# Kernel tuning notes

Hardware: AMD Instinct MI355X
Metric: run time of the kernel (lower is better)

Reference implementation:

```python
import jax, jax.numpy as jnp
import numpy as np
import math

D_MODEL = 1024
NHEAD = 16
HEAD_DIM = D_MODEL // NHEAD  # 64
FREQ = 10000.0


def _rope(x, freq=FREQ):
    # x: [B, H, S, D] with D even. Matches RotaryEmbedding.apply:
    # thetas = exp(-2*log(freq)*(i//2)/D) for i in [0, D/2)
    S, D = x.shape[-2], x.shape[-1]
    pos = jnp.arange(S, dtype=x.dtype)                       # [S]
    idx = jnp.arange(D // 2) // 2                            # floor(i/2)
    thetas = jnp.exp((-2.0 * math.log(freq) / D) * idx.astype(x.dtype))  # [D/2]
    ang = pos[:, None] * thetas[None, :]                     # [S, D/2]
    cos, sin = jnp.cos(ang), jnp.sin(ang)
    x2 = x.reshape(*x.shape[:-1], D // 2, 2)
    x0, x1 = x2[..., 0], x2[..., 1]
    out = jnp.stack([x0 * cos - x1 * sin, x0 * sin + x1 * cos], axis=-1)
    return out.reshape(x.shape)


def setup_inputs() -> dict:
    key = jax.random.key(0)
    k1, k2, k3, k4, k5 = jax.random.split(key, 5)
    B, S = 2, 2048
    scale = 1.0 / math.sqrt(D_MODEL)
    return {
        "embeddings": jax.random.normal(k1, (B, S, D_MODEL), dtype=jnp.float32),
        "W_qkv": jax.random.normal(k2, (D_MODEL, 3 * D_MODEL), dtype=jnp.float32) * scale,
        "b_qkv": jnp.zeros((3 * D_MODEL,), dtype=jnp.float32),
        "W_o": jax.random.normal(k4, (D_MODEL, D_MODEL), dtype=jnp.float32) * scale,
        "b_o": jnp.zeros((D_MODEL,), dtype=jnp.float32),
    }


def reference(embeddings, W_qkv, b_qkv, W_o, b_o):
    B, S, _ = embeddings.shape
    qkv = embeddings @ W_qkv + b_qkv                          # [B,S,3*D]
    q, k, v = jnp.split(qkv, 3, axis=-1)

    def split_heads(t):  # [B,S,D] -> [B,H,S,hd]
        return t.reshape(B, S, NHEAD, HEAD_DIM).transpose(0, 2, 1, 3)

    q, k, v = split_heads(q), split_heads(k), split_heads(v)
    q = _rope(q)
    k = _rope(k)

    scores = jnp.einsum("bhqd,bhkd->bhqk", q, k) / math.sqrt(HEAD_DIM)
    attn = jax.nn.softmax(scores, axis=-1)
    heads = jnp.einsum("bhqk,bhkd->bhqd", attn, v)            # [B,H,S,hd]
    out = heads.transpose(0, 2, 1, 3).reshape(B, S, D_MODEL)
    return out @ W_o + b_o
```

## Files before the change

kernel.cpp:

```cpp
#include <hip/hip_runtime.h>
#include <hip/hip_bf16.h>
#include <math.h>

typedef __bf16 bf16;
typedef __bf16 bf16x4 __attribute__((ext_vector_type(4)));
typedef __bf16 bf16x8 __attribute__((ext_vector_type(8)));
typedef float f32x4 __attribute__((ext_vector_type(4)));

#define DEV static __device__ __forceinline__

#define SS 2048
#define HH 16
#define HD 64

DEV void load_lds16(const bf16* g, bf16* l) {
  __builtin_amdgcn_global_load_lds(
      (const __attribute__((address_space(1))) unsigned int*)g,
      (__attribute__((address_space(3))) unsigned int*)l, 16, 0, 0);
}

#define MFMA(a, b, c) __builtin_amdgcn_mfma_f32_16x16x32_bf16(a, b, c, 0, 0, 0)

__global__ __launch_bounds__(256) void k_prep(
    const float* __restrict__ emb, bf16* __restrict__ Xb,
    const float* __restrict__ Wqkv, bf16* __restrict__ Wqt,
    const float* __restrict__ Wo, bf16* __restrict__ Wot) {
  __shared__ float tt[32][33];
  int bid = blockIdx.x;
  if (bid < 4096) {
    int i = (bid * 256 + threadIdx.x) * 4;
    float4 v = *reinterpret_cast<const float4*>(emb + i);
    bf16x4 o = {(bf16)v.x, (bf16)v.y, (bf16)v.z, (bf16)v.w};
    *reinterpret_cast<bf16x4*>(Xb + i) = o;
    return;
  }
  const float* in;
  bf16* out;
  int R = 1024, C, ctile, rtile;
  if (bid < 7168) {
    in = Wqkv; out = Wqt; C = 3072;
    int idx = bid - 4096; ctile = idx % 96; rtile = idx / 96;
  } else {
    in = Wo; out = Wot; C = 1024;
    int idx = bid - 7168; ctile = idx & 31; rtile = idx >> 5;
  }
  int tx = threadIdx.x & 31, ty = threadIdx.x >> 5;
#pragma unroll
  for (int i = 0; i < 4; ++i)
    tt[ty + 8 * i][tx] = in[(rtile * 32 + ty + 8 * i) * C + ctile * 32 + tx];
  __syncthreads();
#pragma unroll
  for (int i = 0; i < 4; ++i) {
    int oc = ctile * 32 + ty + 8 * i;
    out[oc * R + rtile * 32 + tx] = (bf16)tt[tx][ty + 8 * i];
  }
}

__global__ __launch_bounds__(512) void k_gemm1(
    const bf16* __restrict__ A, const bf16* __restrict__ Bt,
    const float* __restrict__ bias, bf16* __restrict__ Qo,
    bf16* __restrict__ Ko, bf16* __restrict__ Vo) {
  __shared__ bf16 As[2][16384];
  __shared__ bf16 Bs[2][16384];
  int wg = blockIdx.x;
  int xcd = wg & 7, idx = wg >> 3;
  int wgid = xcd * 24 + idx;
  int bm = wgid & 15, bn = wgid >> 4;
  int t = threadIdx.x, w = t >> 6, l = t & 63;
  int wm = w >> 2, wn = w & 3;
  int fr = l & 15, fg = l >> 4;
  const bf16* Ab = A + bm * 256 * 1024;
  const bf16* Bb = Bt + bn * 256 * 1024;
  int trow = t >> 3;
  const bf16* sA = Ab + trow * 1024 + (((t & 7) ^ (trow & 7)) * 8);
  const bf16* sB = Bb + trow * 1024 + (((t & 7) ^ (trow & 7)) * 8);
  int dst0 = (w << 9);
#pragma unroll
  for (int j = 0; j < 4; ++j) {
    load_lds16(sA + j * 65536, &As[0][j * 4096 + dst0]);
    load_lds16(sB + j * 65536, &Bs[0][j * 4096 + dst0]);
  }
  f32x4 acc[8][4];
#pragma unroll
  for (int mi = 0; mi < 8; ++mi)
#pragma unroll
    for (int ni = 0; ni < 4; ++ni) acc[mi][ni] = (f32x4){0.f, 0.f, 0.f, 0.f};
  int xo = fr & 7;
  __syncthreads();
  for (int kt = 0; kt < 16; ++kt) {
    const bf16* Asb = &As[kt & 1][0];
    const bf16* Bsb = &Bs[kt & 1][0];
    bf16* An = &As[(kt & 1) ^ 1][0];
    bf16* Bn = &Bs[(kt & 1) ^ 1][0];
    bool st = kt < 15;
    int ko = (kt + 1) * 64;
    bf16x8 av[4], bv[4];
    if (st) {
      load_lds16(sA + ko, &An[dst0]);
      load_lds16(sA + 65536 + ko, &An[4096 + dst0]);
    }
#pragma unroll
    for (int ni = 0; ni < 4; ++ni)
      bv[ni] = *(const bf16x8*)(Bsb + (wn * 64 + ni * 16 + fr) * 64 + (fg ^ xo) * 8);
#pragma unroll
    for (int mi = 0; mi < 4; ++mi)
      av[mi] = *(const bf16x8*)(Asb + (wm * 128 + mi * 16 + fr) * 64 + (fg ^ xo) * 8);
    __builtin_amdgcn_s_setprio(1);
#pragma unroll
    for (int mi = 0; mi < 4; ++mi)
#pragma unroll
      for (int ni = 0; ni < 4; ++ni)
        acc[mi][ni] = MFMA(av[mi], bv[ni], acc[mi][ni]);
    __builtin_amdgcn_s_setprio(0);
    if (st) {
      load_lds16(sA + 131072 + ko, &An[8192 + dst0]);
      load_lds16(sA + 196608 + ko, &An[12288 + dst0]);
    }
#pragma unroll
    for (int mi = 0; mi < 4; ++mi)
      av[mi] = *(const bf16x8*)(Asb + (wm * 128 + (mi + 4) * 16 + fr) * 64 + (fg ^ xo) * 8);
    __builtin_amdgcn_s_setprio(1);
#pragma unroll
    for (int mi = 0; mi < 4; ++mi)
#pragma unroll
      for (int ni = 0; ni < 4; ++ni)
        acc[mi + 4][ni] = MFMA(av[mi], bv[ni], acc[mi + 4][ni]);
    __builtin_amdgcn_s_setprio(0);
    if (st) {
      load_lds16(sB + ko, &Bn[dst0]);
      load_lds16(sB + 65536 + ko, &Bn[4096 + dst0]);
    }
#pragma unroll
    for (int ni = 0; ni < 4; ++ni)
      bv[ni] = *(const bf16x8*)(Bsb + (wn * 64 + ni * 16 + fr) * 64 + ((4 + fg) ^ xo) * 8);
#pragma unroll
    for (int mi = 0; mi < 4; ++mi)
      av[mi] = *(const bf16x8*)(Asb + (wm * 128 + mi * 16 + fr) * 64 + ((4 + fg) ^ xo) * 8);
    __builtin_amdgcn_s_setprio(1);
#pragma unroll
    for (int mi = 0; mi < 4; ++mi)
#pragma unroll
      for (int ni = 0; ni < 4; ++ni)
        acc[mi][ni] = MFMA(av[mi], bv[ni], acc[mi][ni]);
    __builtin_amdgcn_s_setprio(0);
    if (st) {
      load_lds16(sB + 131072 + ko, &Bn[8192 + dst0]);
      load_lds16(sB + 196608 + ko, &Bn[12288 + dst0]);
    }
#pragma unroll
    for (int mi = 0; mi < 4; ++mi)
      av[mi] = *(const bf16x8*)(Asb + (wm * 128 + (mi + 4) * 16 + fr) * 64 + ((4 + fg) ^ xo) * 8);
    __builtin_amdgcn_s_setprio(1);
#pragma unroll
    for (int mi = 0; mi < 4; ++mi)
#pragma unroll
      for (int ni = 0; ni < 4; ++ni)
        acc[mi + 4][ni] = MFMA(av[mi], bv[ni], acc[mi + 4][ni]);
    __builtin_amdgcn_s_setprio(0);
    __syncthreads();
  }
#pragma unroll
  for (int mi = 0; mi < 8; ++mi)
#pragma unroll
    for (int ni = 0; ni < 4; ++ni) {
      int gc = bn * 256 + wn * 64 + ni * 16 + fr;
      int sec = gc >> 10, cc = gc & 1023;
      bf16* dst = sec == 0 ? Qo : (sec == 1 ? Ko : Vo);
      int h = cc >> 6, d = cc & 63;
      float bb = bias[gc];
      int gr0 = bm * 256 + wm * 128 + mi * 16 + fg * 4;
#pragma unroll
      for (int r = 0; r < 4; ++r) {
        int gr = gr0 + r;
        int b = gr >> 11, s = gr & 2047;
        dst[((b * HH + h) * SS + s) * HD + d] = (bf16)(acc[mi][ni][r] + bb);
      }
    }
}

DEV void gemm_core(const bf16* __restrict__ Ab, const bf16* __restrict__ Bb,
                   bf16* As, bf16* Bs, int w, int l, f32x4 acc[4][4]) {
  int fr = l & 15, fg = l >> 4;
  int wr = (w >> 1) * 64, wc = (w & 1) * 64;
  for (int kt = 0; kt < 16; ++kt) {
#pragma unroll
    for (int i = 0; i < 4; ++i) {
      int blk = w * 4 + i;
      const bf16* ga = Ab + (blk * 8 + (l >> 3)) * 1024 + kt * 64 + (l & 7) * 8;
      const bf16* gb = Bb + (blk * 8 + (l >> 3)) * 1024 + kt * 64 + (l & 7) * 8;
      load_lds16(ga, As + blk * 512);
      load_lds16(gb, Bs + blk * 512);
    }
    __syncthreads();
#pragma unroll
    for (int kk = 0; kk < 2; ++kk) {
      bf16x8 af[4], bfv[4];
#pragma unroll
      for (int mi = 0; mi < 4; ++mi)
        af[mi] = *(const bf16x8*)(As + (wr + mi * 16 + fr) * 64 + kk * 32 + fg * 8);
#pragma unroll
      for (int ni = 0; ni < 4; ++ni)
        bfv[ni] = *(const bf16x8*)(Bs + (wc + ni * 16 + fr) * 64 + kk * 32 + fg * 8);
#pragma unroll
      for (int mi = 0; mi < 4; ++mi)
#pragma unroll
        for (int ni = 0; ni < 4; ++ni)
          acc[mi][ni] = __builtin_amdgcn_mfma_f32_16x16x32_bf16(
              af[mi], bfv[ni], acc[mi][ni], 0, 0, 0);
    }
    __syncthreads();
  }
}

__global__ __launch_bounds__(256) void k_gemm2(
    const bf16* __restrict__ A, const bf16* __restrict__ Bt,
    const float* __restrict__ bias, float* __restrict__ out) {
  __shared__ bf16 As[128 * 64], Bs[128 * 64];
  int wg = blockIdx.x;
  int bm = wg & 31, bn = wg >> 5;
  int t = threadIdx.x, w = t >> 6, l = t & 63;
  f32x4 acc[4][4];
#pragma unroll
  for (int mi = 0; mi < 4; ++mi)
#pragma unroll
    for (int ni = 0; ni < 4; ++ni) acc[mi][ni] = (f32x4){0.f, 0.f, 0.f, 0.f};
  gemm_core(A + bm * 128 * 1024, Bt + bn * 128 * 1024, As, Bs, w, l, acc);
  int fr = l & 15, fg = l >> 4;
  int wr = (w >> 1) * 64, wc = (w & 1) * 64;
#pragma unroll
  for (int mi = 0; mi < 4; ++mi)
#pragma unroll
    for (int ni = 0; ni < 4; ++ni) {
      int gc = bn * 128 + wc + ni * 16 + fr;
      float bb = bias[gc];
      int gr0 = bm * 128 + wr + mi * 16 + fg * 4;
#pragma unroll
      for (int r = 0; r < 4; ++r)
        out[(gr0 + r) * 1024 + gc] = acc[mi][ni][r] + bb;
    }
}

__global__ void k_rope(bf16* __restrict__ Qb, bf16* __restrict__ Kb) {
  int t = blockIdx.x * 256 + threadIdx.x;
  bf16* buf = (t >> 19) ? Kb : Qb;
  float qs = (t >> 19) ? 1.0f : 0.125f;
  int g = t & 524287;
  int j = g & 7;
  int s = (g >> 3) & 2047;
  bf16* p = buf + (long long)g * 8;
  const float CN = -0.28782313662425572f;
  float th0 = __expf(CN * (float)(2 * j));
  float th1 = __expf(CN * (float)(2 * j + 1));
  float sp = (float)s;
  float s0, c0, s1, c1;
  sincosf(sp * th0, &s0, &c0);
  sincosf(sp * th1, &s1, &c1);
  bf16x8 v = *(bf16x8*)p;
  float x[8];
#pragma unroll
  for (int i = 0; i < 8; ++i) x[i] = (float)v[i];
  float o[8];
  o[0] = x[0] * c0 - x[1] * s0; o[1] = x[0] * s0 + x[1] * c0;
  o[2] = x[2] * c0 - x[3] * s0; o[3] = x[2] * s0 + x[3] * c0;
  o[4] = x[4] * c1 - x[5] * s1; o[5] = x[4] * s1 + x[5] * c1;
  o[6] = x[6] * c1 - x[7] * s1; o[7] = x[6] * s1 + x[7] * c1;
  bf16x8 ov;
#pragma unroll
  for (int i = 0; i < 8; ++i) ov[i] = (bf16)(o[i] * qs);
  *(bf16x8*)p = ov;
}

__global__ void k_trV(const bf16* __restrict__ V, bf16* __restrict__ Vt) {
  __shared__ bf16 t[64][66];
  int st = blockIdx.x, bh = blockIdx.y;
  const bf16* vb = V + (long long)bh * SS * HD;
  bf16* ob = Vt + (long long)bh * HD * SS;
  int tx = threadIdx.x & 63, ty = threadIdx.x >> 6;
#pragma unroll
  for (int i = 0; i < 16; ++i)
    t[ty + 4 * i][tx] = vb[(st * 64 + ty + 4 * i) * 64 + tx];
  __syncthreads();
#pragma unroll
  for (int i = 0; i < 16; ++i) {
    int dR = ty + 4 * i;
    ob[dR * SS + st * 64 + tx] = t[tx][dR];
  }
}

__global__ __launch_bounds__(512) void k_attn(
    const bf16* __restrict__ Q, const bf16* __restrict__ K,
    const bf16* __restrict__ Vt, bf16* __restrict__ Hd) {
  __shared__ bf16 KVs[2][8192];
  __shared__ bf16 plds[8][16][72];
  int bid = blockIdx.x;
  int x = bid & 7, rr = bid >> 3;
  int bh = x * 4 + (rr & 3);
  int qt = rr >> 2;
  int b = bh >> 4, h = bh & 15;
  int t = threadIdx.x, w = t >> 6, l = t & 63;
  int fr = l & 15, fg = l >> 4;
  const bf16* Qb = Q + (long long)bh * SS * HD;
  const bf16* Kb = K + (long long)bh * SS * HD;
  const bf16* Vb = Vt + (long long)bh * HD * SS;
  bool isK = w < 4;
  int stride = isK ? 64 : 2048;
  int wrow = (isK ? w : (w - 4)) * 16 + (l >> 3);
  const bf16* src = (isK ? Kb : Vb) + wrow * stride + ((l & 7) ^ (l >> 3)) * 8;
  int adv = isK ? 4096 : 64;
  int dbase = w * 1024;

  int q0 = qt * 128 + w * 16;
  bf16x8 qf0 = *(const bf16x8*)(Qb + (q0 + fr) * 64 + fg * 8);
  bf16x8 qf1 = *(const bf16x8*)(Qb + (q0 + fr) * 64 + 32 + fg * 8);
  f32x4 acc[4];
#pragma unroll
  for (int db = 0; db < 4; ++db) acc[db] = (f32x4){0.f, 0.f, 0.f, 0.f};
  float ssum = 0.f;
  const f32x4 zero = {0.f, 0.f, 0.f, 0.f};
  int xo = fr & 7;

  load_lds16(src, &KVs[0][dbase]);
  load_lds16(src + 8 * stride, &KVs[0][dbase + 512]);
  src += adv;
  __syncthreads();

  for (int it = 0; it < 32; ++it) {
    int buf = it & 1;
    if (it < 31) {
      load_lds16(src, &KVs[buf ^ 1][dbase]);
      load_lds16(src + 8 * stride, &KVs[buf ^ 1][dbase + 512]);
      src += adv;
    }
    const bf16* Ks = &KVs[buf][0];
    const bf16* Vs = &KVs[buf][4096];
    f32x4 stl[4];
    __builtin_amdgcn_s_setprio(1);
#pragma unroll
    for (int ks = 0; ks < 4; ++ks) {
      bf16x8 k0 = *(const bf16x8*)(Ks + (ks * 16 + fr) * 64 + (fg ^ xo) * 8);
      bf16x8 k1 = *(const bf16x8*)(Ks + (ks * 16 + fr) * 64 + ((4 + fg) ^ xo) * 8);
      stl[ks] = MFMA(k0, qf0, zero);
      stl[ks] = MFMA(k1, qf1, stl[ks]);
    }
    __builtin_amdgcn_s_setprio(0);
    float ps = 0.f;
#pragma unroll
    for (int ks = 0; ks < 4; ++ks) {
      bf16x4 pb;
#pragma unroll
      for (int r = 0; r < 4; ++r) {
        float p = __expf(stl[ks][r] - 16.0f);
        ps += p;
        pb[r] = (bf16)p;
      }
      *(bf16x4*)&plds[w][fr][ks * 16 + fg * 4] = pb;
    }
    ssum += ps;
    bf16x8 pf0 = *(const bf16x8*)&plds[w][fr][fg * 8];
    bf16x8 pf1 = *(const bf16x8*)&plds[w][fr][32 + fg * 8];
    __builtin_amdgcn_s_setprio(1);
#pragma unroll
    for (int db = 0; db < 4; ++db) {
      bf16x8 vf0 = *(const bf16x8*)(Vs + (db * 16 + fr) * 64 + (fg ^ xo) * 8);
      bf16x8 vf1 = *(const bf16x8*)(Vs + (db * 16 + fr) * 64 + ((4 + fg) ^ xo) * 8);
      acc[db] = MFMA(vf0, pf0, acc[db]);
      acc[db] = MFMA(vf1, pf1, acc[db]);
    }
    __builtin_amdgcn_s_setprio(0);
    __syncthreads();
  }
  float sv = ssum;
  sv += __shfl_xor(sv, 16);
  sv += __shfl_xor(sv, 32);
  float inv = 1.0f / sv;
  int s = q0 + fr;
#pragma unroll
  for (int db = 0; db < 4; ++db) {
    bf16x4 ob;
#pragma unroll
    for (int r = 0; r < 4; ++r) ob[r] = (bf16)(acc[db][r] * inv);
    *(bf16x4*)(Hd + ((long long)(b * SS + s)) * 1024 + h * 64 + db * 16 + fg * 4) = ob;
  }
}

extern "C" void kernel_launch(void* const* d_in, const int* in_sizes, int n_in,
                              void* d_out, int out_size, void* d_ws, size_t ws_size,
                              hipStream_t stream) {
  const float* emb = (const float*)d_in[0];
  const float* Wqkv = (const float*)d_in[1];
  const float* bqkv = (const float*)d_in[2];
  const float* Wo = (const float*)d_in[3];
  const float* bo = (const float*)d_in[4];
  float* out = (float*)d_out;
  char* ws = (char*)d_ws;
  bf16* Xb  = (bf16*)(ws);
  bf16* Wqt = (bf16*)(ws + 8388608);
  bf16* Wot = (bf16*)(ws + 14680064);
  bf16* Qb  = (bf16*)(ws + 16777216);
  bf16* Kb  = (bf16*)(ws + 25165824);
  bf16* Vb  = (bf16*)(ws + 33554432);
  bf16* Vt  = (bf16*)(ws + 41943040);
  bf16* Hd  = (bf16*)(ws + 50331648);

  hipLaunchKernelGGL(k_prep, dim3(8192), dim3(256), 0, stream, emb, Xb, Wqkv, Wqt, Wo, Wot);
  hipLaunchKernelGGL(k_gemm1, dim3(192), dim3(512), 0, stream, Xb, Wqt, bqkv, Qb, Kb, Vb);
  hipLaunchKernelGGL(k_rope, dim3(4096), dim3(256), 0, stream, Qb, Kb);
  hipLaunchKernelGGL(k_trV, dim3(32, 32), dim3(256), 0, stream, Vb, Vt);
  hipLaunchKernelGGL(k_attn, dim3(512), dim3(512), 0, stream, Qb, Kb, Vt, Hd);
  hipLaunchKernelGGL(k_gemm2, dim3(256), dim3(256), 0, stream, Hd, Wot, bo, out);
}
```

Baseline: 138.4 us.

## Restructure QKV GEMM pipeline, remap tiles per XCD, use exp2 softmax

The QKV GEMM now issues the whole next-stage prefetch up front and places explicit s_barrier, waitcnt and sched_barrier fences around each MFMA phase instead of spreading loads between phases. Block-to-tile mapping is changed so each XCD covers a 4x6 rectangle of tiles, meant to improve L2 reuse. The attention kernel folds log2(e) into the Q scale so it can call exp2f instead of __expf, and it unrolls the KV loop by two with a fixed buffer index. These aim to cut instruction overhead and improve overlap and cache locality, but the extra barriers may add stalls.

```diff
diff --git a/kernel.cpp b/kernel.cpp
--- a/kernel.cpp
+++ b/kernel.cpp
@@ -64,8 +64,8 @@
   __shared__ bf16 Bs[2][16384];
   int wg = blockIdx.x;
   int xcd = wg & 7, idx = wg >> 3;
-  int wgid = xcd * 24 + idx;
-  int bm = wgid & 15, bn = wgid >> 4;
+  int bm = (xcd & 3) * 4 + (idx & 3);
+  int bn = (xcd >> 2) * 6 + (idx >> 2);
   int t = threadIdx.x, w = t >> 6, l = t & 63;
   int wm = w >> 2, wn = w & 3;
   int fr = l & 15, fg = l >> 4;
@@ -75,36 +75,42 @@
   const bf16* sA = Ab + trow * 1024 + (((t & 7) ^ (trow & 7)) * 8);
   const bf16* sB = Bb + trow * 1024 + (((t & 7) ^ (trow & 7)) * 8);
   int dst0 = (w << 9);
-#pragma unroll
-  for (int j = 0; j < 4; ++j) {
-    load_lds16(sA + j * 65536, &As[0][j * 4096 + dst0]);
-    load_lds16(sB + j * 65536, &Bs[0][j * 4096 + dst0]);
-  }
+  int xo = fr & 7;
+
+#define G1_STAGE(buf, ko)                                         \
+  do {                                                            \
+    _Pragma("unroll")                                             \
+    for (int j = 0; j < 4; ++j) {                                 \
+      load_lds16(sA + j * 65536 + (ko), &As[buf][j * 4096 + dst0]); \
+      load_lds16(sB + j * 65536 + (ko), &Bs[buf][j * 4096 + dst0]); \
+    }                                                             \
+  } while (0)
+
   f32x4 acc[8][4];
 #pragma unroll
   for (int mi = 0; mi < 8; ++mi)
 #pragma unroll
     for (int ni = 0; ni < 4; ++ni) acc[mi][ni] = (f32x4){0.f, 0.f, 0.f, 0.f};
-  int xo = fr & 7;
-  __syncthreads();
+
+  G1_STAGE(0, 0);
+  asm volatile("s_waitcnt vmcnt(0)" ::: "memory");
+  __builtin_amdgcn_s_barrier();
+
   for (int kt = 0; kt < 16; ++kt) {
-    const bf16* Asb = &As[kt & 1][0];
-    const bf16* Bsb = &Bs[kt & 1][0];
-    bf16* An = &As[(kt & 1) ^ 1][0];
-    bf16* Bn = &Bs[(kt & 1) ^ 1][0];
-    bool st = kt < 15;
-    int ko = (kt + 1) * 64;
+    int p = kt & 1;
+    const bf16* Asb = &As[p][0];
+    const bf16* Bsb = &Bs[p][0];
+    if (kt < 15) G1_STAGE(p ^ 1, (kt + 1) * 64);
     bf16x8 av[4], bv[4];
-    if (st) {
-      load_lds16(sA + ko, &An[dst0]);
-      load_lds16(sA + 65536 + ko, &An[4096 + dst0]);
-    }
 #pragma unroll
     for (int ni = 0; ni < 4; ++ni)
       bv[ni] = *(const bf16x8*)(Bsb + (wn * 64 + ni * 16 + fr) * 64 + (fg ^ xo) * 8);
 #pragma unroll
     for (int mi = 0; mi < 4; ++mi)
       av[mi] = *(const bf16x8*)(Asb + (wm * 128 + mi * 16 + fr) * 64 + (fg ^ xo) * 8);
+    __builtin_amdgcn_s_barrier();
+    asm volatile("s_waitcnt lgkmcnt(0)" ::: "memory");
+    __builtin_amdgcn_sched_barrier(0);
     __builtin_amdgcn_s_setprio(1);
 #pragma unroll
     for (int mi = 0; mi < 4; ++mi)
@@ -112,13 +118,13 @@
       for (int ni = 0; ni < 4; ++ni)
         acc[mi][ni] = MFMA(av[mi], bv[ni], acc[mi][ni]);
     __builtin_amdgcn_s_setprio(0);
-    if (st) {
-      load_lds16(sA + 131072 + ko, &An[8192 + dst0]);
-      load_lds16(sA + 196608 + ko, &An[12288 + dst0]);
-    }
+    __builtin_amdgcn_s_barrier();
 #pragma unroll
     for (int mi = 0; mi < 4; ++mi)
       av[mi] = *(const bf16x8*)(Asb + (wm * 128 + (mi + 4) * 16 + fr) * 64 + (fg ^ xo) * 8);
+    __builtin_amdgcn_s_barrier();
+    asm volatile("s_waitcnt lgkmcnt(0)" ::: "memory");
+    __builtin_amdgcn_sched_barrier(0);
     __builtin_amdgcn_s_setprio(1);
 #pragma unroll
     for (int mi = 0; mi < 4; ++mi)
@@ -126,16 +132,16 @@
       for (int ni = 0; ni < 4; ++ni)
         acc[mi + 4][ni] = MFMA(av[mi], bv[ni], acc[mi + 4][ni]);
     __builtin_amdgcn_s_setprio(0);
-    if (st) {
-      load_lds16(sB + ko, &Bn[dst0]);
-      load_lds16(sB + 65536 + ko, &Bn[4096 + dst0]);
-    }
+    __builtin_amdgcn_s_barrier();
 #pragma unroll
     for (int ni = 0; ni < 4; ++ni)
       bv[ni] = *(const bf16x8*)(Bsb + (wn * 64 + ni * 16 + fr) * 64 + ((4 + fg) ^ xo) * 8);
 #pragma unroll
     for (int mi = 0; mi < 4; ++mi)
       av[mi] = *(const bf16x8*)(Asb + (wm * 128 + mi * 16 + fr) * 64 + ((4 + fg) ^ xo) * 8);
+    __builtin_amdgcn_s_barrier();
+    asm volatile("s_waitcnt lgkmcnt(0)" ::: "memory");
+    __builtin_amdgcn_sched_barrier(0);
     __builtin_amdgcn_s_setprio(1);
 #pragma unroll
     for (int mi = 0; mi < 4; ++mi)
@@ -143,13 +149,13 @@
       for (int ni = 0; ni < 4; ++ni)
         acc[mi][ni] = MFMA(av[mi], bv[ni], acc[mi][ni]);
     __builtin_amdgcn_s_setprio(0);
-    if (st) {
-      load_lds16(sB + 131072 + ko, &Bn[8192 + dst0]);
-      load_lds16(sB + 196608 + ko, &Bn[12288 + dst0]);
-    }
+    __builtin_amdgcn_s_barrier();
 #pragma unroll
     for (int mi = 0; mi < 4; ++mi)
       av[mi] = *(const bf16x8*)(Asb + (wm * 128 + (mi + 4) * 16 + fr) * 64 + ((4 + fg) ^ xo) * 8);
+    __builtin_amdgcn_s_barrier();
+    asm volatile("s_waitcnt lgkmcnt(0)" ::: "memory");
+    __builtin_amdgcn_sched_barrier(0);
     __builtin_amdgcn_s_setprio(1);
 #pragma unroll
     for (int mi = 0; mi < 4; ++mi)
@@ -157,7 +163,9 @@
       for (int ni = 0; ni < 4; ++ni)
         acc[mi + 4][ni] = MFMA(av[mi], bv[ni], acc[mi + 4][ni]);
     __builtin_amdgcn_s_setprio(0);
-    __syncthreads();
+    asm volatile("s_waitcnt vmcnt(0)" ::: "memory");
+    __builtin_amdgcn_sched_barrier(0);
+    __builtin_amdgcn_s_barrier();
   }
 #pragma unroll
   for (int mi = 0; mi < 8; ++mi)
@@ -176,6 +184,7 @@
         dst[((b * HH + h) * SS + s) * HD + d] = (bf16)(acc[mi][ni][r] + bb);
       }
     }
+#undef G1_STAGE
 }
 
 DEV void gemm_core(const bf16* __restrict__ Ab, const bf16* __restrict__ Bb,
@@ -243,7 +252,7 @@
 __global__ void k_rope(bf16* __restrict__ Qb, bf16* __restrict__ Kb) {
   int t = blockIdx.x * 256 + threadIdx.x;
   bf16* buf = (t >> 19) ? Kb : Qb;
-  float qs = (t >> 19) ? 1.0f : 0.125f;
+  float qs = (t >> 19) ? 1.0f : 0.18033688011112042f;
   int g = t & 524287;
   int j = g & 7;
   int s = (g >> 3) & 2047;
@@ -319,54 +328,61 @@
   const f32x4 zero = {0.f, 0.f, 0.f, 0.f};
   int xo = fr & 7;
 
-  load_lds16(src, &KVs[0][dbase]);
-  load_lds16(src + 8 * stride, &KVs[0][dbase + 512]);
-  src += adv;
+#define ATTN_STAGE(BUF)                              \
+  do {                                               \
+    load_lds16(src, &KVs[BUF][dbase]);               \
+    load_lds16(src + 8 * stride, &KVs[BUF][dbase + 512]); \
+    src += adv;                                      \
+  } while (0)
+
+#define ATTN_COMPUTE(BUF)                                                    \
+  do {                                                                       \
+    const bf16* Ks = &KVs[BUF][0];                                           \
+    const bf16* Vs = &KVs[BUF][4096];                                        \
+    f32x4 stl[4];                                                            \
+    __builtin_amdgcn_s_setprio(1);                                           \
+    _Pragma("unroll")                                                        \
+    for (int ks = 0; ks < 4; ++ks) {                                         \
+      bf16x8 k0 = *(const bf16x8*)(Ks + (ks * 16 + fr) * 64 + (fg ^ xo) * 8);\
+      bf16x8 k1 = *(const bf16x8*)(Ks + (ks * 16 + fr) * 64 + ((4 + fg) ^ xo) * 8); \
+      stl[ks] = MFMA(k0, qf0, zero);                                         \
+      stl[ks] = MFMA(k1, qf1, stl[ks]);                                      \
+    }                                                                        \
+    __builtin_amdgcn_s_setprio(0);                                           \
+    float ps = 0.f;                                                          \
+    _Pragma("unroll")                                                        \
+    for (int ks = 0; ks < 4; ++ks) {                                         \
+      bf16x4 pb;                                                             \
+      _Pragma("unroll")                                                      \
+      for (int r = 0; r < 4; ++r) {                                          \
+        float p = exp2f(stl[ks][r] - 23.083120654223414f);                   \
+        ps += p;                                                             \
+        pb[r] = (bf16)p;                                                     \
+      }                                                                      \
+      *(bf16x4*)&plds[w][fr][ks * 16 + fg * 4] = pb;                         \
+    }                                                                        \
+    ssum += ps;                                                              \
+    bf16x8 pf0 = *(const bf16x8*)&plds[w][fr][fg * 8];                       \
+    bf16x8 pf1 = *(const bf16x8*)&plds[w][fr][32 + fg * 8];                  \
+    __builtin_amdgcn_s_setprio(1);                                           \
+    _Pragma("unroll")                                                        \
+    for (int db = 0; db < 4; ++db) {                                         \
+      bf16x8 vf0 = *(const bf16x8*)(Vs + (db * 16 + fr) * 64 + (fg ^ xo) * 8); \
+      bf16x8 vf1 = *(const bf16x8*)(Vs + (db * 16 + fr) * 64 + ((4 + fg) ^ xo) * 8); \
+      acc[db] = MFMA(vf0, pf0, acc[db]);                                     \
+      acc[db] = MFMA(vf1, pf1, acc[db]);                                     \
+    }                                                                        \
+    __builtin_amdgcn_s_setprio(0);                                           \
+  } while (0)
+
+  ATTN_STAGE(0);
   __syncthreads();
-
-  for (int it = 0; it < 32; ++it) {
-    int buf = it & 1;
-    if (it < 31) {
-      load_lds16(src, &KVs[buf ^ 1][dbase]);
-      load_lds16(src + 8 * stride, &KVs[buf ^ 1][dbase + 512]);
-      src += adv;
-    }
-    const bf16* Ks = &KVs[buf][0];
-    const bf16* Vs = &KVs[buf][4096];
-    f32x4 stl[4];
-    __builtin_amdgcn_s_setprio(1);
-#pragma unroll
-    for (int ks = 0; ks < 4; ++ks) {
-      bf16x8 k0 = *(const bf16x8*)(Ks + (ks * 16 + fr) * 64 + (fg ^ xo) * 8);
-      bf16x8 k1 = *(const bf16x8*)(Ks + (ks * 16 + fr) * 64 + ((4 + fg) ^ xo) * 8);
-      stl[ks] = MFMA(k0, qf0, zero);
-      stl[ks] = MFMA(k1, qf1, stl[ks]);
-    }
-    __builtin_amdgcn_s_setprio(0);
-    float ps = 0.f;
-#pragma unroll
-    for (int ks = 0; ks < 4; ++ks) {
-      bf16x4 pb;
-#pragma unroll
-      for (int r = 0; r < 4; ++r) {
-        float p = __expf(stl[ks][r] - 16.0f);
-        ps += p;
-        pb[r] = (bf16)p;
-      }
-      *(bf16x4*)&plds[w][fr][ks * 16 + fg * 4] = pb;
-    }
-    ssum += ps;
-    bf16x8 pf0 = *(const bf16x8*)&plds[w][fr][fg * 8];
-    bf16x8 pf1 = *(const bf16x8*)&plds[w][fr][32 + fg * 8];
-    __builtin_amdgcn_s_setprio(1);
-#pragma unroll
-    for (int db = 0; db < 4; ++db) {
-      bf16x8 vf0 = *(const bf16x8*)(Vs + (db * 16 + fr) * 64 + (fg ^ xo) * 8);
-      bf16x8 vf1 = *(const bf16x8*)(Vs + (db * 16 + fr) * 64 + ((4 + fg) ^ xo) * 8);
-      acc[db] = MFMA(vf0, pf0, acc[db]);
-      acc[db] = MFMA(vf1, pf1, acc[db]);
-    }
-    __builtin_amdgcn_s_setprio(0);
+  for (int it = 0; it < 32; it += 2) {
+    ATTN_STAGE(1);
+    ATTN_COMPUTE(0);
+    __syncthreads();
+    if (it < 30) ATTN_STAGE(0);
+    ATTN_COMPUTE(1);
     __syncthreads();
   }
   float sv = ssum;
@@ -381,6 +397,8 @@
     for (int r = 0; r < 4; ++r) ob[r] = (bf16)(acc[db][r] * inv);
     *(bf16x4*)(Hd + ((long long)(b * SS + s)) * 1024 + h * 64 + db * 16 + fg * 4) = ob;
   }
+#undef ATTN_STAGE
+#undef ATTN_COMPUTE
 }
 
 extern "C" void kernel_launch(void* const* d_in, const int* in_sizes, int n_in,
```

Result: slower. 143.1 us (+3.4%).
